# Performance work log

Measured on AMD Instinct MI355X. Metric: run time of the kernel, lower is better.

The kernel has to match this reference:

```python
import jax, jax.numpy as jnp
import numpy as np

N_NODES = 100000
N_EDGES = 1000000
F_IN = 64
F_HID = 64
F_OUT = 2
NUM_GRAPHS = 64


def setup_inputs() -> dict:
    key = jax.random.key(0)
    ks = jax.random.split(key, 8)
    x = jax.random.normal(ks[0], (N_NODES, F_IN), dtype=jnp.float32)
    edge_index = jax.random.randint(ks[1], (2, N_EDGES), 0, N_NODES, dtype=jnp.int32)
    batch = jnp.sort(jax.random.randint(ks[2], (N_NODES,), 0, NUM_GRAPHS, dtype=jnp.int32))
    s1 = 1.0 / np.sqrt(F_IN)
    s2 = 1.0 / np.sqrt(F_HID)
    W1 = jax.random.normal(ks[3], (F_IN, F_HID), dtype=jnp.float32) * s1
    W2 = jax.random.normal(ks[4], (F_HID, F_HID), dtype=jnp.float32) * s2
    W3 = jax.random.normal(ks[5], (F_HID, F_HID), dtype=jnp.float32) * s2
    Wlin = jax.random.normal(ks[6], (F_HID, F_OUT), dtype=jnp.float32) * s2
    return {
        "x": x, "edge_index": edge_index, "batch": batch,
        "W1": W1, "b1": jnp.zeros((F_HID,), jnp.float32),
        "W2": W2, "b2": jnp.zeros((F_HID,), jnp.float32),
        "W3": W3, "b3": jnp.zeros((F_HID,), jnp.float32),
        "Wlin": Wlin, "blin": jnp.zeros((F_OUT,), jnp.float32),
    }


def _gcn_norm(edge_index, n_nodes):
    # add self-loops, compute symmetric D^-1/2 (A+I) D^-1/2 edge weights
    loops = jnp.arange(n_nodes, dtype=edge_index.dtype)
    src = jnp.concatenate([edge_index[0], loops])  # message source j
    dst = jnp.concatenate([edge_index[1], loops])  # aggregation target i
    deg = jax.ops.segment_sum(jnp.ones_like(dst, dtype=jnp.float32), dst,
                              num_segments=n_nodes)
    dinv = jnp.where(deg > 0, jax.lax.rsqrt(deg), 0.0)
    norm = dinv[src] * dinv[dst]  # [E+N]
    return src, dst, norm


def _gcn_conv(h, W, b, src, dst, norm, n_nodes):
    h = h @ W                                    # [N, F] dense transform first (PyG order)
    msg = h[src] * norm[:, None]                 # gather + scale  [E+N, F]
    agg = jax.ops.segment_sum(msg, dst, num_segments=n_nodes)
    return agg + b


def reference(x, edge_index, batch, W1, b1, W2, b2, W3, b3, Wlin, blin):
    n = x.shape[0]
    src, dst, norm = _gcn_norm(edge_index, n)
    h = jax.nn.relu(_gcn_conv(x, W1, b1, src, dst, norm, n))
    h = jax.nn.relu(_gcn_conv(h, W2, b2, src, dst, norm, n))
    h = _gcn_conv(h, W3, b3, src, dst, norm, n)
    # global mean pool over graphs
    sums = jax.ops.segment_sum(h, batch, num_segments=NUM_GRAPHS)        # [G, F]
    cnts = jax.ops.segment_sum(jnp.ones((n,), jnp.float32), batch,
                               num_segments=NUM_GRAPHS)
    pooled = sums / jnp.maximum(cnts, 1.0)[:, None]
    # dropout(p=0.1) is identity in eval mode
    return pooled @ Wlin + blin
```

## Files before the change

kernel.cpp:

```cpp
#include <hip/hip_runtime.h>

#define FDIM 64

typedef unsigned short u16;
typedef unsigned int u32;
typedef float v2f __attribute__((ext_vector_type(2)));

__device__ __forceinline__ u16 f2bf(float x) {
    unsigned int u = __float_as_uint(x);
    return (u16)((u + 0x7fff + ((u >> 16) & 1)) >> 16);
}
__device__ __forceinline__ float bf2f(u16 h) {
    return __uint_as_float(((unsigned int)h) << 16);
}
__device__ __forceinline__ u32 pk_fp8x4(float a, float b, float c, float d) {
    u32 p = __builtin_amdgcn_cvt_pk_fp8_f32(a, b, 0, false);
    p = __builtin_amdgcn_cvt_pk_fp8_f32(c, d, p, true);
    return p;
}


template <bool BF16IN>
__device__ __forceinline__ void mm_tile64(
    const void* __restrict__ ain, const float* __restrict__ bias, int do_relu,
    u32* __restrict__ t, int n, int blk,
    float (*__restrict__ As)[FDIM + 1], float* __restrict__ Ws)
{
    int tid = threadIdx.x;
    int r0 = blk * 64;

    #pragma unroll
    for (int i = 0; i < 4; ++i) {
        int idx = tid + 256 * i;
        int r = idx >> 4;
        int kq = idx & 15;
        float4 v = make_float4(0.f, 0.f, 0.f, 0.f);
        int R = r0 + r;
        if (R < n) {
            if (BF16IN) {
                ushort4 h = ((const ushort4*)ain)[(size_t)R * 16 + kq];
                v.x = bf2f(h.x); v.y = bf2f(h.y); v.z = bf2f(h.z); v.w = bf2f(h.w);
            } else {
                v = ((const float4*)ain)[(size_t)R * 16 + kq];
            }
            if (bias != nullptr) {
                float4 b = ((const float4*)bias)[kq];
                v.x += b.x; v.y += b.y; v.z += b.z; v.w += b.w;
            }
            if (do_relu) {
                v.x = fmaxf(v.x, 0.f); v.y = fmaxf(v.y, 0.f);
                v.z = fmaxf(v.z, 0.f); v.w = fmaxf(v.w, 0.f);
            }
        }
        As[r][kq * 4 + 0] = v.x;
        As[r][kq * 4 + 1] = v.y;
        As[r][kq * 4 + 2] = v.z;
        As[r][kq * 4 + 3] = v.w;
    }
    __syncthreads();

    int rq = tid >> 4;
    int cq = tid & 15;
    float acc[4][4];
    #pragma unroll
    for (int i = 0; i < 4; ++i)
        #pragma unroll
        for (int j = 0; j < 4; ++j) acc[i][j] = 0.f;

    const float4* Ws4 = (const float4*)Ws;
    #pragma unroll 4
    for (int k = 0; k < FDIM; ++k) {
        float4 w = Ws4[k * 16 + cq];
        float a[4];
        #pragma unroll
        for (int i = 0; i < 4; ++i) a[i] = As[rq * 4 + i][k];
        #pragma unroll
        for (int i = 0; i < 4; ++i) {
            acc[i][0] = fmaf(a[i], w.x, acc[i][0]);
            acc[i][1] = fmaf(a[i], w.y, acc[i][1]);
            acc[i][2] = fmaf(a[i], w.z, acc[i][2]);
            acc[i][3] = fmaf(a[i], w.w, acc[i][3]);
        }
    }

    #pragma unroll
    for (int i = 0; i < 4; ++i) {
        int R = r0 + rq * 4 + i;
        if (R < n)
            t[(size_t)R * 16 + cq] =
                pk_fp8x4(acc[i][0], acc[i][1], acc[i][2], acc[i][3]);
    }
}

__global__ __launch_bounds__(256) void k_matmul_h(
    const u16* __restrict__ ain, const float* __restrict__ Wm,
    const float* __restrict__ bias, u32* __restrict__ t, int n)
{
    __shared__ float As[64][FDIM + 1];
    __shared__ float Ws[FDIM * FDIM];
    int tid = threadIdx.x;
    #pragma unroll
    for (int i = 0; i < 4; ++i)
        ((float4*)Ws)[tid + 256 * i] = ((const float4*)Wm)[tid + 256 * i];
    mm_tile64<true>(ain, bias, 1, t, n, blockIdx.x, As, Ws);
}


__global__ __launch_bounds__(256) void k_mm_fill(
    const float* __restrict__ x, const float* __restrict__ W1,
    u32* __restrict__ t,
    const int* __restrict__ src, const int* __restrict__ dst,
    int* __restrict__ cnt, int* __restrict__ csr,
    int n, int E, int cap, int mm_blocks, int fill_chunks)
{
    __shared__ float As[64][FDIM + 1];
    __shared__ float Ws[FDIM * FDIM];

    if ((int)blockIdx.x < mm_blocks) {
        int tid = threadIdx.x;
        #pragma unroll
        for (int i = 0; i < 4; ++i)
            ((float4*)Ws)[tid + 256 * i] = ((const float4*)W1)[tid + 256 * i];
        mm_tile64<false>(x, nullptr, 0, t, n, blockIdx.x, As, Ws);
        return;
    }
    int gb = blockIdx.x - mm_blocks;
    int part = blockIdx.x & 7;
    int chunk = gb >> 3;
    int psz = n >> 3;
    int lo = psz * part;
    int hi = (part == 7) ? n : lo + psz;
    int per = (E + fill_chunks - 1) / fill_chunks;
    int ebeg = chunk * per;
    int eend = ebeg + per; if (eend > E) eend = E;

    int e = ebeg + (int)threadIdx.x;
    for (; e + 768 < eend; e += 1024) {
        int d0 = __builtin_nontemporal_load(&dst[e]);
        int d1 = __builtin_nontemporal_load(&dst[e + 256]);
        int d2 = __builtin_nontemporal_load(&dst[e + 512]);
        int d3 = __builtin_nontemporal_load(&dst[e + 768]);
        int s0 = __builtin_nontemporal_load(&src[e]);
        int s1 = __builtin_nontemporal_load(&src[e + 256]);
        int s2 = __builtin_nontemporal_load(&src[e + 512]);
        int s3 = __builtin_nontemporal_load(&src[e + 768]);
        bool k0 = (d0 >= lo) && (d0 < hi);
        bool k1 = (d1 >= lo) && (d1 < hi);
        bool k2 = (d2 >= lo) && (d2 < hi);
        bool k3 = (d3 >= lo) && (d3 < hi);
        int p0 = 0, p1 = 0, p2 = 0, p3 = 0;
        if (k0) p0 = atomicAdd(&cnt[d0], 1);
        if (k1) p1 = atomicAdd(&cnt[d1], 1);
        if (k2) p2 = atomicAdd(&cnt[d2], 1);
        if (k3) p3 = atomicAdd(&cnt[d3], 1);
        if (k0 && p0 < cap) csr[(size_t)d0 * cap + p0] = s0;
        if (k1 && p1 < cap) csr[(size_t)d1 * cap + p1] = s1;
        if (k2 && p2 < cap) csr[(size_t)d2 * cap + p2] = s2;
        if (k3 && p3 < cap) csr[(size_t)d3 * cap + p3] = s3;
    }
    for (; e < eend; e += 256) {
        int d = dst[e];
        if (d >= lo && d < hi) {
            int p = atomicAdd(&cnt[d], 1);
            if (p < cap) csr[(size_t)d * cap + p] = src[e];
        }
    }
}


__global__ __launch_bounds__(256) void k_aggregate(
    const int* __restrict__ cnt, const int* __restrict__ csr,
    const u32* __restrict__ t, float* __restrict__ aggf,
    uint2* __restrict__ aggh, int outf32, int n, int cap)
{
    int tid = threadIdx.x;
    long long gw = ((long long)blockIdx.x * 256 + tid) >> 6;
    int lane = tid & 63;
    int sub = lane >> 4;
    int li  = lane & 15;
    long long il = gw * 4 + sub;
    if (il >= n) return;
    int i = (int)il;

    int deg = cnt[i];
    float di = rsqrtf((float)deg + 1.0f);
    int m = deg < cap ? deg : cap;

    u32 sp = t[(size_t)i * 16 + li];
    v2f s0 = __builtin_amdgcn_cvt_pk_f32_fp8(sp, false);
    v2f s1 = __builtin_amdgcn_cvt_pk_f32_fp8(sp, true);
    float4 A0 = make_float4(s0.x * di, s0.y * di, s1.x * di, s1.y * di);
    float4 A1 = make_float4(0.f, 0.f, 0.f, 0.f);
    float4 A2 = make_float4(0.f, 0.f, 0.f, 0.f);
    float4 A3 = make_float4(0.f, 0.f, 0.f, 0.f);

    const int* row = csr + (size_t)i * cap;
    int nbase = sub << 4;

    for (int c0 = 0; c0 < m; c0 += 16) {
        int cm = m - c0; if (cm > 16) cm = 16;
        int sv = 0; float dvv = 0.f;
        if (li < cm) { sv = row[c0 + li]; dvv = rsqrtf((float)cnt[sv] + 1.0f); }
        int k = 0;
        for (; k + 8 <= cm; k += 8) {
            int jv[8]; float dj[8]; u32 v[8];
            #pragma unroll
            for (int u = 0; u < 8; ++u) {
                jv[u] = __shfl(sv, nbase + k + u);
                dj[u] = __shfl(dvv, nbase + k + u);
            }
            #pragma unroll
            for (int u = 0; u < 8; ++u) v[u] = t[(size_t)jv[u] * 16 + li];
            #pragma unroll
            for (int u = 0; u < 8; ++u) {
                v2f x0 = __builtin_amdgcn_cvt_pk_f32_fp8(v[u], false);
                v2f x1 = __builtin_amdgcn_cvt_pk_f32_fp8(v[u], true);
                float4* Ap = (u & 3) == 0 ? &A0 : (u & 3) == 1 ? &A1 :
                             (u & 3) == 2 ? &A2 : &A3;
                Ap->x = fmaf(x0.x, dj[u], Ap->x);
                Ap->y = fmaf(x0.y, dj[u], Ap->y);
                Ap->z = fmaf(x1.x, dj[u], Ap->z);
                Ap->w = fmaf(x1.y, dj[u], Ap->w);
            }
        }
        if (k + 4 <= cm) {
            int jv[4]; float dj[4]; u32 v[4];
            #pragma unroll
            for (int u = 0; u < 4; ++u) {
                jv[u] = __shfl(sv, nbase + k + u);
                dj[u] = __shfl(dvv, nbase + k + u);
            }
            #pragma unroll
            for (int u = 0; u < 4; ++u) v[u] = t[(size_t)jv[u] * 16 + li];
            #pragma unroll
            for (int u = 0; u < 4; ++u) {
                v2f x0 = __builtin_amdgcn_cvt_pk_f32_fp8(v[u], false);
                v2f x1 = __builtin_amdgcn_cvt_pk_f32_fp8(v[u], true);
                float4* Ap = u == 0 ? &A0 : u == 1 ? &A1 : u == 2 ? &A2 : &A3;
                Ap->x = fmaf(x0.x, dj[u], Ap->x);
                Ap->y = fmaf(x0.y, dj[u], Ap->y);
                Ap->z = fmaf(x1.x, dj[u], Ap->z);
                Ap->w = fmaf(x1.y, dj[u], Ap->w);
            }
            k += 4;
        }
        for (; k < cm; ++k) {
            int j = __shfl(sv, nbase + k);
            float dj = __shfl(dvv, nbase + k);
            u32 vv = t[(size_t)j * 16 + li];
            v2f x0 = __builtin_amdgcn_cvt_pk_f32_fp8(vv, false);
            v2f x1 = __builtin_amdgcn_cvt_pk_f32_fp8(vv, true);
            A0.x = fmaf(x0.x, dj, A0.x);
            A0.y = fmaf(x0.y, dj, A0.y);
            A0.z = fmaf(x1.x, dj, A0.z);
            A0.w = fmaf(x1.y, dj, A0.w);
        }
    }

    float4 O;
    O.x = ((A0.x + A1.x) + (A2.x + A3.x)) * di;
    O.y = ((A0.y + A1.y) + (A2.y + A3.y)) * di;
    O.z = ((A0.z + A1.z) + (A2.z + A3.z)) * di;
    O.w = ((A0.w + A1.w) + (A2.w + A3.w)) * di;
    if (outf32) {
        ((float4*)aggf)[(size_t)i * 16 + li] = O;
    } else {
        uint2 pk;
        pk.x = ((u32)f2bf(O.x)) | (((u32)f2bf(O.y)) << 16);
        pk.y = ((u32)f2bf(O.z)) | (((u32)f2bf(O.w)) << 16);
        aggh[(size_t)i * 16 + li] = pk;
    }
}


__global__ __launch_bounds__(256) void k_pool1(
    const float* __restrict__ agg, const int* __restrict__ batch,
    float* __restrict__ partial, int n)
{
    int g = blockIdx.x >> 3;
    int part = blockIdx.x & 7;
    int tid = threadIdx.x;

    int lo = 0, hi = n;
    while (lo < hi) { int mid = (lo + hi) >> 1; if (batch[mid] < g) lo = mid + 1; else hi = mid; }
    int start = lo;
    hi = n;
    while (lo < hi) { int mid = (lo + hi) >> 1; if (batch[mid] <= g) lo = mid + 1; else hi = mid; }
    int end = lo;

    int f = tid & 63, r = tid >> 6;
    float s = 0.f;
    for (int i = start + part * 4 + r; i < end; i += 32)
        s += agg[(size_t)i * 64 + f];

    __shared__ float red[4][64];
    red[r][f] = s;
    __syncthreads();
    if (tid < 64)
        partial[((size_t)g * 8 + part) * 64 + tid] =
            red[0][tid] + red[1][tid] + red[2][tid] + red[3][tid];
}

__global__ __launch_bounds__(64) void k_pool2(
    const float* __restrict__ partial, const int* __restrict__ batch,
    const float* __restrict__ b3, const float* __restrict__ Wlin,
    const float* __restrict__ blin, float* __restrict__ out,
    int n, int fout)
{
    int g = blockIdx.x;
    int tid = threadIdx.x;

    int lo = 0, hi = n;
    while (lo < hi) { int mid = (lo + hi) >> 1; if (batch[mid] < g) lo = mid + 1; else hi = mid; }
    int start = lo;
    hi = n;
    while (lo < hi) { int mid = (lo + hi) >> 1; if (batch[mid] <= g) lo = mid + 1; else hi = mid; }
    int cnt = lo - start;

    __shared__ float pooled[64];
    float v = 0.f;
    #pragma unroll
    for (int p = 0; p < 8; ++p) v += partial[((size_t)g * 8 + p) * 64 + tid];
    pooled[tid] = (cnt > 0) ? (v / (float)cnt + b3[tid]) : 0.f;
    __syncthreads();
    if (tid < fout) {
        float o = blin[tid];
        for (int k = 0; k < 64; ++k) o += pooled[k] * Wlin[k * fout + tid];
        out[(size_t)g * fout + tid] = o;
    }
}


extern "C" void kernel_launch(void* const* d_in, const int* in_sizes, int n_in,
                              void* d_out, int out_size, void* d_ws, size_t ws_size,
                              hipStream_t stream) {
    const float* x     = (const float*)d_in[0];
    const int*   ei    = (const int*)d_in[1];
    const int*   batch = (const int*)d_in[2];
    const float* W1 = (const float*)d_in[3];
    const float* b1 = (const float*)d_in[4];
    const float* W2 = (const float*)d_in[5];
    const float* b2 = (const float*)d_in[6];
    const float* W3 = (const float*)d_in[7];
    const float* b3 = (const float*)d_in[8];
    const float* Wl = (const float*)d_in[9];
    const float* bl = (const float*)d_in[10];

    int n = in_sizes[0] / 64;
    int E = in_sizes[1] / 2;
    int fout = in_sizes[10];
    int ngraphs = out_size / fout;

    const int* srcp = ei;
    const int* dstp = ei + E;

    float* ws   = (float*)d_ws;
    float* agg  = ws;
    u32*   t    = (u32*)(agg + (size_t)n * 64);
    float* partial = (float*)(t + (size_t)n * 16);
    int* cnt    = (int*)(partial + 64 * 8 * 64);
    int* csr    = cnt + n;

    size_t fixed = (size_t)n * 64 * 4 + (size_t)n * 16 * 4 +
                   64 * 8 * 64 * 4 + (size_t)n * 4;
    int cap = 64;
    while (cap > 32 && fixed + (size_t)n * cap * 4 > ws_size) cap -= 8;

    int nb_ag = (int)((((long long)(n + 3) / 4) * 64 + 255) / 256);
    int mm_blocks = (((n + 63) / 64 + 7) / 8) * 8;
    int fill_chunks = 128;

    hipMemsetAsync(cnt, 0, (size_t)n * sizeof(int), stream);
    k_mm_fill<<<mm_blocks + 8 * fill_chunks, 256, 0, stream>>>(
        x, W1, t, srcp, dstp, cnt, csr, n, E, cap, mm_blocks, fill_chunks);

    k_aggregate<<<nb_ag, 256, 0, stream>>>(cnt, csr, t, agg, (uint2*)agg, 0, n, cap);
    k_matmul_h<<<mm_blocks, 256, 0, stream>>>((const u16*)agg, W2, b1, t, n);
    k_aggregate<<<nb_ag, 256, 0, stream>>>(cnt, csr, t, agg, (uint2*)agg, 0, n, cap);
    k_matmul_h<<<mm_blocks, 256, 0, stream>>>((const u16*)agg, W3, b2, t, n);
    k_aggregate<<<nb_ag, 256, 0, stream>>>(cnt, csr, t, agg, (uint2*)agg, 1, n, cap);

    k_pool1<<<ngraphs * 8, 256, 0, stream>>>(agg, batch, partial, n);
    k_pool2<<<ngraphs, 64, 0, stream>>>(partial, batch, b3, Wl, bl, (float*)d_out, n, fout);
}
```

Measured before the change: 287.4 us.

## Split fp8 feature table into column halves and map halves to XCD groups

```diff
diff --git a/kernel.cpp b/kernel.cpp
--- a/kernel.cpp
+++ b/kernel.cpp
@@ -23,7 +23,7 @@
 template <bool BF16IN>
 __device__ __forceinline__ void mm_tile64(
     const void* __restrict__ ain, const float* __restrict__ bias, int do_relu,
-    u32* __restrict__ t, int n, int blk,
+    u32* __restrict__ t0, u32* __restrict__ t1, int n, int blk,
     float (*__restrict__ As)[FDIM + 1], float* __restrict__ Ws)
 {
     int tid = threadIdx.x;
@@ -83,18 +83,21 @@
         }
     }
 
+    u32* th = (cq < 8) ? t0 : t1;
+    int co = cq & 7;
     #pragma unroll
     for (int i = 0; i < 4; ++i) {
         int R = r0 + rq * 4 + i;
         if (R < n)
-            t[(size_t)R * 16 + cq] =
+            th[(size_t)R * 8 + co] =
                 pk_fp8x4(acc[i][0], acc[i][1], acc[i][2], acc[i][3]);
     }
 }
 
 __global__ __launch_bounds__(256) void k_matmul_h(
     const u16* __restrict__ ain, const float* __restrict__ Wm,
-    const float* __restrict__ bias, u32* __restrict__ t, int n)
+    const float* __restrict__ bias, u32* __restrict__ t0, u32* __restrict__ t1,
+    int n)
 {
     __shared__ float As[64][FDIM + 1];
     __shared__ float Ws[FDIM * FDIM];
@@ -102,13 +105,13 @@
     #pragma unroll
     for (int i = 0; i < 4; ++i)
         ((float4*)Ws)[tid + 256 * i] = ((const float4*)Wm)[tid + 256 * i];
-    mm_tile64<true>(ain, bias, 1, t, n, blockIdx.x, As, Ws);
+    mm_tile64<true>(ain, bias, 1, t0, t1, n, blockIdx.x, As, Ws);
 }
 
 
 __global__ __launch_bounds__(256) void k_mm_fill(
     const float* __restrict__ x, const float* __restrict__ W1,
-    u32* __restrict__ t,
+    u32* __restrict__ t0, u32* __restrict__ t1,
     const int* __restrict__ src, const int* __restrict__ dst,
     int* __restrict__ cnt, int* __restrict__ csr,
     int n, int E, int cap, int mm_blocks, int fill_chunks)
@@ -121,7 +124,7 @@
         #pragma unroll
         for (int i = 0; i < 4; ++i)
             ((float4*)Ws)[tid + 256 * i] = ((const float4*)W1)[tid + 256 * i];
-        mm_tile64<false>(x, nullptr, 0, t, n, blockIdx.x, As, Ws);
+        mm_tile64<false>(x, nullptr, 0, t0, t1, n, blockIdx.x, As, Ws);
         return;
     }
     int gb = blockIdx.x - mm_blocks;
@@ -170,105 +173,91 @@
 
 __global__ __launch_bounds__(256) void k_aggregate(
     const int* __restrict__ cnt, const int* __restrict__ csr,
-    const u32* __restrict__ t, float* __restrict__ aggf,
-    uint2* __restrict__ aggh, int outf32, int n, int cap)
-{
-    int tid = threadIdx.x;
-    long long gw = ((long long)blockIdx.x * 256 + tid) >> 6;
+    const u32* __restrict__ t0, const u32* __restrict__ t1,
+    float* __restrict__ aggf, uint2* __restrict__ aggh,
+    int outf32, int n, int cap, int npc)
+{
+    int tid = threadIdx.x;
+    int xcd = blockIdx.x & 7;
+    int h = xcd >> 2;
+    int cid = ((int)blockIdx.x >> 3) * 4 + (xcd & 3);
+    int i0 = cid * npc;
+    if (i0 >= n) return;
+    int i1 = i0 + npc; if (i1 > n) i1 = n;
+
+    const u32* th = h ? t1 : t0;
+    int w = tid >> 6;
     int lane = tid & 63;
-    int sub = lane >> 4;
-    int li  = lane & 15;
-    long long il = gw * 4 + sub;
-    if (il >= n) return;
-    int i = (int)il;
-
-    int deg = cnt[i];
-    float di = rsqrtf((float)deg + 1.0f);
-    int m = deg < cap ? deg : cap;
-
-    u32 sp = t[(size_t)i * 16 + li];
-    v2f s0 = __builtin_amdgcn_cvt_pk_f32_fp8(sp, false);
-    v2f s1 = __builtin_amdgcn_cvt_pk_f32_fp8(sp, true);
-    float4 A0 = make_float4(s0.x * di, s0.y * di, s1.x * di, s1.y * di);
-    float4 A1 = make_float4(0.f, 0.f, 0.f, 0.f);
-    float4 A2 = make_float4(0.f, 0.f, 0.f, 0.f);
-    float4 A3 = make_float4(0.f, 0.f, 0.f, 0.f);
-
-    const int* row = csr + (size_t)i * cap;
-    int nbase = sub << 4;
-
-    for (int c0 = 0; c0 < m; c0 += 16) {
-        int cm = m - c0; if (cm > 16) cm = 16;
-        int sv = 0; float dvv = 0.f;
-        if (li < cm) { sv = row[c0 + li]; dvv = rsqrtf((float)cnt[sv] + 1.0f); }
-        int k = 0;
-        for (; k + 8 <= cm; k += 8) {
-            int jv[8]; float dj[8]; u32 v[8];
-            #pragma unroll
-            for (int u = 0; u < 8; ++u) {
-                jv[u] = __shfl(sv, nbase + k + u);
-                dj[u] = __shfl(dvv, nbase + k + u);
-            }
-            #pragma unroll
-            for (int u = 0; u < 8; ++u) v[u] = t[(size_t)jv[u] * 16 + li];
-            #pragma unroll
-            for (int u = 0; u < 8; ++u) {
-                v2f x0 = __builtin_amdgcn_cvt_pk_f32_fp8(v[u], false);
-                v2f x1 = __builtin_amdgcn_cvt_pk_f32_fp8(v[u], true);
-                float4* Ap = (u & 3) == 0 ? &A0 : (u & 3) == 1 ? &A1 :
-                             (u & 3) == 2 ? &A2 : &A3;
-                Ap->x = fmaf(x0.x, dj[u], Ap->x);
-                Ap->y = fmaf(x0.y, dj[u], Ap->y);
-                Ap->z = fmaf(x1.x, dj[u], Ap->z);
-                Ap->w = fmaf(x1.y, dj[u], Ap->w);
-            }
-        }
-        if (k + 4 <= cm) {
-            int jv[4]; float dj[4]; u32 v[4];
-            #pragma unroll
-            for (int u = 0; u < 4; ++u) {
-                jv[u] = __shfl(sv, nbase + k + u);
-                dj[u] = __shfl(dvv, nbase + k + u);
-            }
-            #pragma unroll
-            for (int u = 0; u < 4; ++u) v[u] = t[(size_t)jv[u] * 16 + li];
-            #pragma unroll
-            for (int u = 0; u < 4; ++u) {
-                v2f x0 = __builtin_amdgcn_cvt_pk_f32_fp8(v[u], false);
-                v2f x1 = __builtin_amdgcn_cvt_pk_f32_fp8(v[u], true);
-                float4* Ap = u == 0 ? &A0 : u == 1 ? &A1 : u == 2 ? &A2 : &A3;
-                Ap->x = fmaf(x0.x, dj[u], Ap->x);
-                Ap->y = fmaf(x0.y, dj[u], Ap->y);
-                Ap->z = fmaf(x1.x, dj[u], Ap->z);
-                Ap->w = fmaf(x1.y, dj[u], Ap->w);
-            }
-            k += 4;
-        }
-        for (; k < cm; ++k) {
-            int j = __shfl(sv, nbase + k);
-            float dj = __shfl(dvv, nbase + k);
-            u32 vv = t[(size_t)j * 16 + li];
-            v2f x0 = __builtin_amdgcn_cvt_pk_f32_fp8(vv, false);
-            v2f x1 = __builtin_amdgcn_cvt_pk_f32_fp8(vv, true);
-            A0.x = fmaf(x0.x, dj, A0.x);
-            A0.y = fmaf(x0.y, dj, A0.y);
-            A0.z = fmaf(x1.x, dj, A0.z);
-            A0.w = fmaf(x1.y, dj, A0.w);
-        }
-    }
-
-    float4 O;
-    O.x = ((A0.x + A1.x) + (A2.x + A3.x)) * di;
-    O.y = ((A0.y + A1.y) + (A2.y + A3.y)) * di;
-    O.z = ((A0.z + A1.z) + (A2.z + A3.z)) * di;
-    O.w = ((A0.w + A1.w) + (A2.w + A3.w)) * di;
-    if (outf32) {
-        ((float4*)aggf)[(size_t)i * 16 + li] = O;
-    } else {
-        uint2 pk;
-        pk.x = ((u32)f2bf(O.x)) | (((u32)f2bf(O.y)) << 16);
-        pk.y = ((u32)f2bf(O.z)) | (((u32)f2bf(O.w)) << 16);
-        aggh[(size_t)i * 16 + li] = pk;
+    int sub = lane >> 3;
+    int li = lane & 7;
+    int nbase = sub << 3;
+
+    for (int i = i0 + w * 8 + sub; i < i1; i += 32) {
+        int deg = cnt[i];
+        float di = rsqrtf((float)deg + 1.0f);
+        int m = deg < cap ? deg : cap;
+
+        u32 sp = th[(size_t)i * 8 + li];
+        v2f s0 = __builtin_amdgcn_cvt_pk_f32_fp8(sp, false);
+        v2f s1 = __builtin_amdgcn_cvt_pk_f32_fp8(sp, true);
+        float4 A0 = make_float4(s0.x * di, s0.y * di, s1.x * di, s1.y * di);
+        float4 A1 = make_float4(0.f, 0.f, 0.f, 0.f);
+
+        const int* row = csr + (size_t)i * cap;
+        for (int c0 = 0; c0 < m; c0 += 8) {
+            int cm = m - c0; if (cm > 8) cm = 8;
+            int sv = 0; float dvv = 0.f;
+            if (li < cm) {
+                sv = __builtin_nontemporal_load(&row[c0 + li]);
+                dvv = rsqrtf((float)cnt[sv] + 1.0f);
+            }
+            if (cm == 8) {
+                int jv[8]; float dj[8]; u32 v[8];
+                #pragma unroll
+                for (int u = 0; u < 8; ++u) {
+                    jv[u] = __shfl(sv, nbase + u);
+                    dj[u] = __shfl(dvv, nbase + u);
+                }
+                #pragma unroll
+                for (int u = 0; u < 8; ++u) v[u] = th[(size_t)jv[u] * 8 + li];
+                #pragma unroll
+                for (int u = 0; u < 8; ++u) {
+                    v2f x0 = __builtin_amdgcn_cvt_pk_f32_fp8(v[u], false);
+                    v2f x1 = __builtin_amdgcn_cvt_pk_f32_fp8(v[u], true);
+                    float4* Ap = (u & 1) ? &A1 : &A0;
+                    Ap->x = fmaf(x0.x, dj[u], Ap->x);
+                    Ap->y = fmaf(x0.y, dj[u], Ap->y);
+                    Ap->z = fmaf(x1.x, dj[u], Ap->z);
+                    Ap->w = fmaf(x1.y, dj[u], Ap->w);
+                }
+            } else {
+                for (int k = 0; k < cm; ++k) {
+                    int j = __shfl(sv, nbase + k);
+                    float dj = __shfl(dvv, nbase + k);
+                    u32 vv = th[(size_t)j * 8 + li];
+                    v2f x0 = __builtin_amdgcn_cvt_pk_f32_fp8(vv, false);
+                    v2f x1 = __builtin_amdgcn_cvt_pk_f32_fp8(vv, true);
+                    A0.x = fmaf(x0.x, dj, A0.x);
+                    A0.y = fmaf(x0.y, dj, A0.y);
+                    A0.z = fmaf(x1.x, dj, A0.z);
+                    A0.w = fmaf(x1.y, dj, A0.w);
+                }
+            }
+        }
+
+        float4 O;
+        O.x = (A0.x + A1.x) * di;
+        O.y = (A0.y + A1.y) * di;
+        O.z = (A0.z + A1.z) * di;
+        O.w = (A0.w + A1.w) * di;
+        if (outf32) {
+            ((float4*)aggf)[(size_t)i * 16 + h * 8 + li] = O;
+        } else {
+            uint2 pk;
+            pk.x = ((u32)f2bf(O.x)) | (((u32)f2bf(O.y)) << 16);
+            pk.y = ((u32)f2bf(O.z)) | (((u32)f2bf(O.w)) << 16);
+            aggh[(size_t)i * 16 + h * 8 + li] = pk;
+        }
     }
 }
 
@@ -356,8 +345,9 @@
 
     float* ws   = (float*)d_ws;
     float* agg  = ws;
-    u32*   t    = (u32*)(agg + (size_t)n * 64);
-    float* partial = (float*)(t + (size_t)n * 16);
+    u32*   t0   = (u32*)(agg + (size_t)n * 64);
+    u32*   t1   = t0 + (size_t)n * 8;
+    float* partial = (float*)(t1 + (size_t)n * 8);
     int* cnt    = (int*)(partial + 64 * 8 * 64);
     int* csr    = cnt + n;
 
@@ -366,19 +356,21 @@
     int cap = 64;
     while (cap > 32 && fixed + (size_t)n * cap * 4 > ws_size) cap -= 8;
 
-    int nb_ag = (int)((((long long)(n + 3) / 4) * 64 + 255) / 256);
     int mm_blocks = (((n + 63) / 64 + 7) / 8) * 8;
     int fill_chunks = 128;
+    int nchunks = 1024;
+    int npc = (n + nchunks - 1) / nchunks;
+    int ag_grid = 8 * (nchunks / 4);
 
     hipMemsetAsync(cnt, 0, (size_t)n * sizeof(int), stream);
     k_mm_fill<<<mm_blocks + 8 * fill_chunks, 256, 0, stream>>>(
-        x, W1, t, srcp, dstp, cnt, csr, n, E, cap, mm_blocks, fill_chunks);
-
-    k_aggregate<<<nb_ag, 256, 0, stream>>>(cnt, csr, t, agg, (uint2*)agg, 0, n, cap);
-    k_matmul_h<<<mm_blocks, 256, 0, stream>>>((const u16*)agg, W2, b1, t, n);
-    k_aggregate<<<nb_ag, 256, 0, stream>>>(cnt, csr, t, agg, (uint2*)agg, 0, n, cap);
-    k_matmul_h<<<mm_blocks, 256, 0, stream>>>((const u16*)agg, W3, b2, t, n);
-    k_aggregate<<<nb_ag, 256, 0, stream>>>(cnt, csr, t, agg, (uint2*)agg, 1, n, cap);
+        x, W1, t0, t1, srcp, dstp, cnt, csr, n, E, cap, mm_blocks, fill_chunks);
+
+    k_aggregate<<<ag_grid, 256, 0, stream>>>(cnt, csr, t0, t1, agg, (uint2*)agg, 0, n, cap, npc);
+    k_matmul_h<<<mm_blocks, 256, 0, stream>>>((const u16*)agg, W2, b1, t0, t1, n);
+    k_aggregate<<<ag_grid, 256, 0, stream>>>(cnt, csr, t0, t1, agg, (uint2*)agg, 0, n, cap, npc);
+    k_matmul_h<<<mm_blocks, 256, 0, stream>>>((const u16*)agg, W3, b2, t0, t1, n);
+    k_aggregate<<<ag_grid, 256, 0, stream>>>(cnt, csr, t0, t1, agg, (uint2*)agg, 1, n, cap, npc);
 
     k_pool1<<<ngraphs * 8, 256, 0, stream>>>(agg, batch, partial, n);
     k_pool2<<<ngraphs, 64, 0, stream>>>(partial, batch, b3, Wl, bl, (float*)d_out, n, fout);
```

New measurement: 382.8 us. +33.2%, slower.
